# Kernel optimization log

Hardware: AMD Instinct MI355X
Metric: run time of the kernel (lower is better)

Reference implementation:

```python
import jax, jax.numpy as jnp
import numpy as np

B, V, FC, J = 1024, 5023, 9976, 5
NSHAPE, NEXP = 100, 50
PARENTS = np.array([-1, 0, 1, 1, 1])
NECK_CHAIN = np.array([1, 0])  # neck then its parent (global)


def batch_rodrigues(rv):
    # rv: [N,3] axis-angle -> [N,3,3] rotation matrices
    angle = jnp.linalg.norm(rv + 1e-8, axis=1, keepdims=True)  # [N,1]
    n = rv / angle
    rx, ry, rz = n[:, 0], n[:, 1], n[:, 2]
    z = jnp.zeros_like(rx)
    K = jnp.stack([z, -rz, ry, rz, z, -rx, -ry, rx, z], axis=1).reshape(-1, 3, 3)
    s = jnp.sin(angle)[..., None]
    c = jnp.cos(angle)[..., None]
    I = jnp.eye(3, dtype=rv.dtype)
    return I + s * K + (1.0 - c) * jnp.matmul(K, K)


def setup_inputs() -> dict:
    key = jax.random.key(0)
    ks = jax.random.split(key, 16)
    inp = {}
    inp["shape_params"] = jax.random.normal(ks[0], (B, NSHAPE), jnp.float32)
    inp["expression_params"] = jax.random.normal(ks[1], (B, NEXP), jnp.float32)
    inp["pose_params"] = jax.random.normal(ks[2], (B, 6), jnp.float32) * 0.2
    inp["v_template"] = jax.random.normal(ks[3], (V, 3), jnp.float32) * 0.1
    inp["shapedirs"] = jax.random.normal(ks[4], (V, 3, NSHAPE + NEXP), jnp.float32) * 0.01
    inp["posedirs"] = jax.random.normal(ks[5], (36, V * 3), jnp.float32) * 0.01
    Jr = jax.random.uniform(ks[6], (J, V), jnp.float32)
    inp["J_regressor"] = Jr / Jr.sum(1, keepdims=True)
    Wl = jax.random.uniform(ks[7], (V, J), jnp.float32)
    inp["lbs_weights"] = Wl / Wl.sum(1, keepdims=True)
    inp["neck_pose"] = jnp.zeros((1, 3), jnp.float32)
    inp["eye_pose"] = jnp.zeros((1, 6), jnp.float32)
    inp["faces"] = jax.random.randint(ks[8], (FC, 3), 0, V)
    inp["lmk_faces_idx"] = jax.random.randint(ks[9], (51,), 0, FC)
    b = jax.random.uniform(ks[10], (51, 3), jnp.float32)
    inp["lmk_bary_coords"] = b / b.sum(-1, keepdims=True)
    inp["dynamic_lmk_faces_idx"] = jax.random.randint(ks[11], (79, 17), 0, FC)
    db = jax.random.uniform(ks[12], (79, 17, 3), jnp.float32)
    inp["dynamic_lmk_bary_coords"] = db / db.sum(-1, keepdims=True)
    inp["full_lmk_faces_idx"] = jax.random.randint(ks[13], (68,), 0, FC)
    fb = jax.random.uniform(ks[14], (68, 3), jnp.float32)
    inp["full_lmk_bary_coords"] = fb / fb.sum(-1, keepdims=True)
    return inp


def reference(shape_params, expression_params, pose_params, v_template, shapedirs,
              posedirs, J_regressor, lbs_weights, neck_pose, eye_pose, faces,
              lmk_faces_idx, lmk_bary_coords, dynamic_lmk_faces_idx,
              dynamic_lmk_bary_coords, full_lmk_faces_idx, full_lmk_bary_coords):
    b = shape_params.shape[0]
    dt = shape_params.dtype
    betas = jnp.concatenate([shape_params, expression_params], 1)  # [B,150]
    full_pose = jnp.concatenate([pose_params[:, :3],
                                 jnp.broadcast_to(neck_pose, (b, 3)),
                                 pose_params[:, 3:],
                                 jnp.broadcast_to(eye_pose, (b, 6))], 1)  # [B,15]
    # shape/expression blendshapes
    v_shaped = v_template[None] + jnp.einsum('bl,vcl->bvc', betas, shapedirs)  # [B,V,3]
    joints = jnp.einsum('jv,bvc->bjc', J_regressor, v_shaped)  # [B,J,3]
    rot_mats = batch_rodrigues(full_pose.reshape(-1, 3)).reshape(b, J, 3, 3)
    ident = jnp.eye(3, dtype=dt)
    pose_feature = (rot_mats[:, 1:] - ident).reshape(b, -1)  # [B,36]
    v_posed = v_shaped + (pose_feature @ posedirs).reshape(b, V, 3)
    # kinematic chain of rigid transforms
    rel_joints = joints.at[:, 1:].add(-joints[:, PARENTS[1:]])
    tmat = jnp.concatenate([rot_mats, rel_joints[..., None]], -1)  # [B,J,3,4]
    bottom = jnp.broadcast_to(jnp.array([0., 0., 0., 1.], dt), (b, J, 1, 4))
    tmat = jnp.concatenate([tmat, bottom], 2)  # [B,J,4,4]
    chains = [tmat[:, 0]]
    for i in range(1, J):
        chains.append(chains[PARENTS[i]] @ tmat[:, i])
    transforms = jnp.stack(chains, 1)  # [B,J,4,4]
    joints_h = jnp.concatenate([joints, jnp.zeros((b, J, 1), dt)], -1)
    rel_tf = transforms - jnp.pad(transforms @ joints_h[..., None],
                                  ((0, 0), (0, 0), (0, 0), (3, 0)))
    # linear blend skinning
    T = jnp.einsum('vj,bjmn->bvmn', lbs_weights, rel_tf)  # [B,V,4,4]
    v_h = jnp.concatenate([v_posed, jnp.ones((b, V, 1), dt)], -1)
    vertices = jnp.einsum('bvmn,bvn->bvm', T, v_h)[..., :3]  # [B,V,3]
    # dynamic contour landmark selection via neck kinematic chain yaw
    aa = full_pose.reshape(b, J, 3)[:, NECK_CHAIN]  # [B,2,3]
    rch = batch_rodrigues(aa.reshape(-1, 3)).reshape(b, 2, 3, 3)
    rel_rot = rch[:, 1] @ rch[:, 0]  # loop order: R_global @ R_neck
    sy = jnp.sqrt(rel_rot[:, 0, 0] ** 2 + rel_rot[:, 1, 0] ** 2)
    yang = jnp.arctan2(-rel_rot[:, 2, 0], sy) * (180.0 / np.pi)
    y = jnp.round(jnp.minimum(yang, 39.0)).astype(jnp.int32)
    neg = y < 0
    big = y < -39
    y = jnp.where(neg, jnp.where(big, 78, 39 - y), y)
    dyn_faces = dynamic_lmk_faces_idx[y]   # [B,17]
    dyn_bary = dynamic_lmk_bary_coords[y]  # [B,17,3]
    lf = jnp.concatenate([dyn_faces,
                          jnp.broadcast_to(lmk_faces_idx[None], (b,) + lmk_faces_idx.shape)], 1)
    lb = jnp.concatenate([dyn_bary,
                          jnp.broadcast_to(lmk_bary_coords[None], (b,) + lmk_bary_coords.shape)], 1)

    def _lmk(verts, lfaces, lbary):
        tri = faces[lfaces]  # [B,L,3] vertex ids
        lv = jax.vmap(lambda v, t: v[t])(verts, tri)  # [B,L,3,3]
        return jnp.einsum('blfc,blf->blc', lv, lbary)

    landmarks2d = _lmk(vertices, lf, lb)  # [B,68,3]
    full_lf = jnp.broadcast_to(full_lmk_faces_idx[None], (b,) + full_lmk_faces_idx.shape)
    full_lb = jnp.broadcast_to(full_lmk_bary_coords[None], (b,) + full_lmk_bary_coords.shape)
    landmarks3d = _lmk(vertices, full_lf, full_lb)  # [B,68,3]
    return vertices, landmarks2d, landmarks3d
```

## Files before the change

kernel.cpp:

```cpp
#include <hip/hip_runtime.h>
#include <math.h>

#define BATCH 1024
#define NV 5023
#define NJ 5
#define K1 150
#define K2 36
#define KTOT 186
#define MCOLS (NV*3)
#define NCHUNK 80
#define CHUNKV 63

typedef __attribute__((ext_vector_type(4))) float floatx4;

#define WS_JSD     0
#define WS_RELTF   2272
#define WS_Y       63712
#define WS_AT      64736
#define WS_PARTIAL 64736

__device__ __forceinline__ void rodrigues(const float* rv, float* R) {
  const float ex = rv[0]+1e-8f, ey = rv[1]+1e-8f, ez = rv[2]+1e-8f;
  const float angle = sqrtf(ex*ex + ey*ey + ez*ez);
  const float inv = 1.0f/angle;
  const float nx = rv[0]*inv, ny = rv[1]*inv, nz = rv[2]*inv;
  const float s = sinf(angle), c = cosf(angle);
  const float omc = 1.0f - c;
  R[0] = 1.0f - omc*(ny*ny+nz*nz);
  R[1] = -s*nz + omc*nx*ny;
  R[2] =  s*ny + omc*nx*nz;
  R[3] =  s*nz + omc*nx*ny;
  R[4] = 1.0f - omc*(nx*nx+nz*nz);
  R[5] = -s*nx + omc*ny*nz;
  R[6] = -s*ny + omc*nx*nz;
  R[7] =  s*nx + omc*ny*nz;
  R[8] = 1.0f - omc*(nx*nx+ny*ny);
}

__launch_bounds__(512)
__global__ void k1_jsd_partial(const float* __restrict__ jreg, const float* __restrict__ shdirs,
                               const float* __restrict__ vtemp, float* __restrict__ partial) {
  const int chunk = blockIdx.x;
  const int t = threadIdx.x;
  if (t >= 453) return;
  const int v0 = chunk*CHUNKV;
  const int v1 = (v0 + CHUNKV < NV) ? v0 + CHUNKV : NV;
  float acc[5] = {0.f,0.f,0.f,0.f,0.f};
  if (t < 450) {
    for (int v = v0; v < v1; ++v) {
      const float sv = shdirs[(size_t)v*450 + t];
      #pragma unroll
      for (int j=0;j<5;++j) acc[j] = fmaf(jreg[j*NV + v], sv, acc[j]);
    }
  } else {
    const int c = t - 450;
    for (int v = v0; v < v1; ++v) {
      const float sv = vtemp[v*3 + c];
      #pragma unroll
      for (int j=0;j<5;++j) acc[j] = fmaf(jreg[j*NV + v], sv, acc[j]);
    }
  }
  #pragma unroll
  for (int j=0;j<5;++j)
    partial[(size_t)(chunk*NJ + j)*453 + t] = acc[j];
}

__launch_bounds__(256)
__global__ void k1b_jsd_reduce(const float* __restrict__ partial, float* __restrict__ jsd) {
  const int i = blockIdx.x*256 + threadIdx.x;
  if (i >= NJ*453) return;
  float s = 0.0f;
  for (int c = 0; c < NCHUNK; ++c) s += partial[(size_t)c*(NJ*453) + i];
  jsd[i] = s;
}

__launch_bounds__(256)
__global__ void k2_pose(const float* __restrict__ shape, const float* __restrict__ expr,
                        const float* __restrict__ pose, const float* __restrict__ neck,
                        const float* __restrict__ eye, const float* __restrict__ jsd,
                        float* __restrict__ At, float* __restrict__ reltf,
                        int* __restrict__ yidx) {
  const int b = blockIdx.x*256 + threadIdx.x;
  if (b >= BATCH) return;

  float fp[15];
  fp[0]=pose[b*6+0]; fp[1]=pose[b*6+1]; fp[2]=pose[b*6+2];
  fp[3]=neck[0];     fp[4]=neck[1];     fp[5]=neck[2];
  fp[6]=pose[b*6+3]; fp[7]=pose[b*6+4]; fp[8]=pose[b*6+5];
  #pragma unroll
  for (int i=0;i<6;++i) fp[9+i] = eye[i];

  float R[5][9];
  #pragma unroll
  for (int j=0;j<5;++j) rodrigues(&fp[j*3], R[j]);

  for (int l=0;l<100;++l) At[(size_t)l*BATCH + b] = shape[(size_t)b*100 + l];
  for (int l=0;l<50;++l)  At[(size_t)(100+l)*BATCH + b] = expr[(size_t)b*50 + l];
  #pragma unroll
  for (int jj=0;jj<4;++jj)
    #pragma unroll
    for (int rc=0;rc<9;++rc)
      At[(size_t)(K1 + jj*9 + rc)*BATCH + b] = R[1+jj][rc] - ((rc==0||rc==4||rc==8)?1.0f:0.0f);

  float jac[15];
  #pragma unroll
  for (int jc=0;jc<15;++jc) jac[jc] = jsd[(jc/3)*453 + 450 + (jc%3)];
  for (int l=0;l<150;++l) {
    const float bv = (l<100) ? shape[(size_t)b*100+l] : expr[(size_t)b*50 + (l-100)];
    #pragma unroll
    for (int jc=0;jc<15;++jc)
      jac[jc] = fmaf(jsd[(jc/3)*453 + (jc%3)*150 + l], bv, jac[jc]);
  }

  float C[5][12];
  #pragma unroll
  for (int r=0;r<3;++r) {
    C[0][r*4+0]=R[0][r*3+0]; C[0][r*4+1]=R[0][r*3+1]; C[0][r*4+2]=R[0][r*3+2];
    C[0][r*4+3]=jac[r];
  }
  const int par[5] = {-1,0,1,1,1};
  #pragma unroll
  for (int i=1;i<5;++i) {
    const int p = par[i];
    const float rj0 = jac[i*3+0]-jac[p*3+0];
    const float rj1 = jac[i*3+1]-jac[p*3+1];
    const float rj2 = jac[i*3+2]-jac[p*3+2];
    #pragma unroll
    for (int r=0;r<3;++r) {
      const float c0=C[p][r*4+0], c1=C[p][r*4+1], c2=C[p][r*4+2], c3=C[p][r*4+3];
      C[i][r*4+0] = c0*R[i][0] + c1*R[i][3] + c2*R[i][6];
      C[i][r*4+1] = c0*R[i][1] + c1*R[i][4] + c2*R[i][7];
      C[i][r*4+2] = c0*R[i][2] + c1*R[i][5] + c2*R[i][8];
      C[i][r*4+3] = c0*rj0 + c1*rj1 + c2*rj2 + c3;
    }
  }

  float* rt = reltf + (size_t)b*60;
  #pragma unroll
  for (int j=0;j<5;++j) {
    const float jx=jac[j*3+0], jy=jac[j*3+1], jz=jac[j*3+2];
    #pragma unroll
    for (int r=0;r<3;++r) {
      const float m0=C[j][r*4+0], m1=C[j][r*4+1], m2=C[j][r*4+2], m3=C[j][r*4+3];
      rt[j*12+r*4+0]=m0; rt[j*12+r*4+1]=m1; rt[j*12+r*4+2]=m2;
      rt[j*12+r*4+3]=m3 - (m0*jx + m1*jy + m2*jz);
    }
  }

  const float c00=R[1][0], c10=R[1][3], c20=R[1][6];
  const float r00 = R[0][0]*c00 + R[0][1]*c10 + R[0][2]*c20;
  const float r10 = R[0][3]*c00 + R[0][4]*c10 + R[0][5]*c20;
  const float r20 = R[0][6]*c00 + R[0][7]*c10 + R[0][8]*c20;
  const float sy = sqrtf(r00*r00 + r10*r10);
  const float yang = atan2f(-r20, sy) * 57.29577951308232f;
  int y = (int)rintf(fminf(yang, 39.0f));
  if (y < 0) y = (y < -39) ? 78 : (39 - y);
  yidx[b] = y;
}

template<int KL, bool POSE>
__device__ __forceinline__ void chunk_body(int k0, int t, int vl, int aoff, int m0,
    const float* __restrict__ At, const float* __restrict__ shdirs,
    const float* __restrict__ pdirs, float* shB,
    float (&acc)[2][8][3]) {
  __syncthreads();
  if (!POSE) {
    constexpr int Q = KL/2;
    constexpr int TOT = 384*Q;
    for (int i = t; i < TOT; i += 512) {
      const int q  = i % Q;
      const int ml = i / Q;
      const int v  = ml/3, c = ml - v*3;
      int m = m0 + ml; if (m > MCOLS-1) m = MCOLS-1;
      const float2 f = *reinterpret_cast<const float2*>(shdirs + (size_t)m*K1 + k0 + 2*q);
      shB[(2*q)*512 + v*4 + c]   = f.x;
      shB[(2*q+1)*512 + v*4 + c] = f.y;
    }
  } else {
    constexpr int TOT = 384*KL;
    for (int i = t; i < TOT; i += 512) {
      const int kk = i / 384;
      const int ml = i - kk*384;
      const int v  = ml/3, c = ml - v*3;
      int m = m0 + ml; if (m > MCOLS-1) m = MCOLS-1;
      shB[kk*512 + v*4 + c] = pdirs[(size_t)(k0 - K1 + kk)*MCOLS + m];
    }
  }
  __syncthreads();
  #pragma unroll 2
  for (int kk = 0; kk < KL; ++kk) {
    const float* ap = At + (size_t)(k0+kk)*BATCH + aoff;
    float as[8];
    #pragma unroll
    for (int i=0;i<8;++i) as[i] = ap[i];
    const floatx4 bv0 = *reinterpret_cast<const floatx4*>(shB + kk*512 + vl*4);
    const floatx4 bv1 = *reinterpret_cast<const floatx4*>(shB + kk*512 + 256 + vl*4);
    #pragma unroll
    for (int i=0;i<8;++i) {
      acc[0][i][0] = fmaf(as[i], bv0[0], acc[0][i][0]);
      acc[0][i][1] = fmaf(as[i], bv0[1], acc[0][i][1]);
      acc[0][i][2] = fmaf(as[i], bv0[2], acc[0][i][2]);
      acc[1][i][0] = fmaf(as[i], bv1[0], acc[1][i][0]);
      acc[1][i][1] = fmaf(as[i], bv1[1], acc[1][i][1]);
      acc[1][i][2] = fmaf(as[i], bv1[2], acc[1][i][2]);
    }
  }
}

__launch_bounds__(512)
__global__ void k3_valu(const float* __restrict__ At, const float* __restrict__ shdirs,
                        const float* __restrict__ pdirs, const float* __restrict__ vtemp,
                        const float* __restrict__ lbsw, const float* __restrict__ reltf,
                        float* __restrict__ vout) {
  __shared__ float shB[32*512];
  __shared__ float sRel[64*60];

  const int t  = threadIdx.x;
  const int vl = t & 63;
  const int bg = t >> 6;
  const int v0 = blockIdx.x * 128;
  const int b0 = blockIdx.y * 64;
  const int m0 = v0*3;
  const int aoff = __builtin_amdgcn_readfirstlane(b0 + bg*8);

  for (int i = t; i < 64*60; i += 512)
    sRel[i] = reltf[(size_t)b0*60 + i];

  float acc[2][8][3] = {};

  #pragma unroll 1
  for (int ch = 0; ch < 4; ++ch)
    chunk_body<32,false>(ch*32, t, vl, aoff, m0, At, shdirs, pdirs, shB, acc);
  chunk_body<22,false>(128, t, vl, aoff, m0, At, shdirs, pdirs, shB, acc);
  chunk_body<32,true >(150, t, vl, aoff, m0, At, shdirs, pdirs, shB, acc);
  chunk_body<4, true >(182, t, vl, aoff, m0, At, shdirs, pdirs, shB, acc);

  #pragma unroll
  for (int p=0;p<2;++p) {
    const int v = v0 + vl + p*64;
    if (v >= NV) continue;
    float w5[5];
    #pragma unroll
    for (int j=0;j<5;++j) w5[j] = lbsw[(size_t)v*5 + j];
    const float tx = vtemp[(size_t)v*3+0];
    const float ty = vtemp[(size_t)v*3+1];
    const float tz = vtemp[(size_t)v*3+2];
    #pragma unroll
    for (int i=0;i<8;++i) {
      const int bl = bg*8 + i;
      const float* rl = &sRel[bl*60];
      const float vx = acc[p][i][0]+tx, vy = acc[p][i][1]+ty, vz = acc[p][i][2]+tz;
      float o[3];
      #pragma unroll
      for (int r=0;r<3;++r) {
        float a0=0.f,a1=0.f,a2=0.f,a3=0.f;
        #pragma unroll
        for (int j=0;j<5;++j) {
          a0 = fmaf(w5[j], rl[j*12+r*4+0], a0);
          a1 = fmaf(w5[j], rl[j*12+r*4+1], a1);
          a2 = fmaf(w5[j], rl[j*12+r*4+2], a2);
          a3 = fmaf(w5[j], rl[j*12+r*4+3], a3);
        }
        o[r] = fmaf(a0, vx, fmaf(a1, vy, fmaf(a2, vz, a3)));
      }
      float* dst = vout + ((size_t)(b0+bl)*NV + v)*3;
      dst[0]=o[0]; dst[1]=o[1]; dst[2]=o[2];
    }
  }
}

__launch_bounds__(192)
__global__ void k4_landmarks(const float* __restrict__ verts, const int* __restrict__ faces,
                             const int* __restrict__ lmkf, const float* __restrict__ lmkb,
                             const int* __restrict__ dynf, const float* __restrict__ dynb,
                             const int* __restrict__ fullf, const float* __restrict__ fullb,
                             const int* __restrict__ yidx, float* __restrict__ out2d,
                             float* __restrict__ out3d) {
  const int b = blockIdx.x;
  const int t = threadIdx.x;
  if (t >= 136) return;
  const int which = t >= 68;
  const int i = which ? (t-68) : t;
  int fidx; float bw0,bw1,bw2;
  if (!which) {
    if (i < 17) {
      const int y = yidx[b];
      fidx = dynf[y*17 + i];
      const float* p = dynb + ((size_t)y*17 + i)*3;
      bw0=p[0]; bw1=p[1]; bw2=p[2];
    } else {
      fidx = lmkf[i-17];
      const float* p = lmkb + (size_t)(i-17)*3;
      bw0=p[0]; bw1=p[1]; bw2=p[2];
    }
  } else {
    fidx = fullf[i];
    const float* p = fullb + (size_t)i*3;
    bw0=p[0]; bw1=p[1]; bw2=p[2];
  }
  const int t0 = faces[fidx*3+0], t1 = faces[fidx*3+1], t2 = faces[fidx*3+2];
  const float* vb = verts + (size_t)b*NV*3;
  float* dst = (which ? out3d : out2d) + ((size_t)b*68 + i)*3;
  #pragma unroll
  for (int c=0;c<3;++c)
    dst[c] = vb[(size_t)t0*3+c]*bw0 + vb[(size_t)t1*3+c]*bw1 + vb[(size_t)t2*3+c]*bw2;
}

extern "C" void kernel_launch(void* const* d_in, const int* in_sizes, int n_in,
                              void* d_out, int out_size, void* d_ws, size_t ws_size,
                              hipStream_t stream) {
  const float* shape = (const float*)d_in[0];
  const float* expr  = (const float*)d_in[1];
  const float* pose  = (const float*)d_in[2];
  const float* vtemp = (const float*)d_in[3];
  const float* shdirs= (const float*)d_in[4];
  const float* pdirs = (const float*)d_in[5];
  const float* jreg  = (const float*)d_in[6];
  const float* lbsw  = (const float*)d_in[7];
  const float* neck  = (const float*)d_in[8];
  const float* eye   = (const float*)d_in[9];
  const int*   faces = (const int*)d_in[10];
  const int*   lmkf  = (const int*)d_in[11];
  const float* lmkb  = (const float*)d_in[12];
  const int*   dynf  = (const int*)d_in[13];
  const float* dynb  = (const float*)d_in[14];
  const int*   fullf = (const int*)d_in[15];
  const float* fullb = (const float*)d_in[16];

  float* wsf = (float*)d_ws;
  float* jsd     = wsf + WS_JSD;
  float* reltf   = wsf + WS_RELTF;
  int*   yidx    = (int*)(wsf + WS_Y);
  float* At      = wsf + WS_AT;
  float* partial = wsf + WS_PARTIAL;

  float* vout  = (float*)d_out;
  float* out2d = vout + (size_t)BATCH*NV*3;
  float* out3d = out2d + (size_t)BATCH*68*3;

  hipLaunchKernelGGL(k1_jsd_partial, dim3(NCHUNK), dim3(512), 0, stream,
                     jreg, shdirs, vtemp, partial);
  hipLaunchKernelGGL(k1b_jsd_reduce, dim3(9), dim3(256), 0, stream, partial, jsd);
  hipLaunchKernelGGL(k2_pose, dim3(4), dim3(256), 0, stream,
                     shape, expr, pose, neck, eye, jsd, At, reltf, yidx);
  hipLaunchKernelGGL(k3_valu, dim3((NV + 127)/128, BATCH/64), dim3(512), 0, stream,
                     At, shdirs, pdirs, vtemp, lbsw, reltf, vout);
  hipLaunchKernelGGL(k4_landmarks, dim3(BATCH), dim3(192), 0, stream,
                     vout, faces, lmkf, lmkb, dynf, dynb, fullf, fullb, yidx, out2d, out3d);
}
```

Before: 220.0 us.

## Retile vertex GEMM kernel to 64 vertices x 16 batches per thread

The main blendshape/LBS kernel now uses 256-thread blocks covering 64 vertices, with each thread handling one vertex across 16 batch rows instead of two vertices across 8. This shrinks shared memory (padded row stride, no staged rel-transform table), doubles the grid and adds a launch_bounds occupancy hint. The aim is better occupancy and fewer redundant shared-memory B loads. In exchange, each thread reads twice as many A scalars per k, and the skinning epilogue now reads the transforms straight from global memory.

```diff
diff --git a/kernel.cpp b/kernel.cpp
--- a/kernel.cpp
+++ b/kernel.cpp
@@ -158,75 +158,66 @@
   yidx[b] = y;
 }
 
+#define SROW 260
+
 template<int KL, bool POSE>
 __device__ __forceinline__ void chunk_body(int k0, int t, int vl, int aoff, int m0,
     const float* __restrict__ At, const float* __restrict__ shdirs,
-    const float* __restrict__ pdirs, float* shB,
-    float (&acc)[2][8][3]) {
+    const float* __restrict__ pdirs, float* shB, float (&acc)[16][3]) {
   __syncthreads();
   if (!POSE) {
     constexpr int Q = KL/2;
-    constexpr int TOT = 384*Q;
-    for (int i = t; i < TOT; i += 512) {
+    constexpr int TOT = 192*Q;
+    for (int i = t; i < TOT; i += 256) {
       const int q  = i % Q;
       const int ml = i / Q;
       const int v  = ml/3, c = ml - v*3;
       int m = m0 + ml; if (m > MCOLS-1) m = MCOLS-1;
       const float2 f = *reinterpret_cast<const float2*>(shdirs + (size_t)m*K1 + k0 + 2*q);
-      shB[(2*q)*512 + v*4 + c]   = f.x;
-      shB[(2*q+1)*512 + v*4 + c] = f.y;
+      shB[(2*q)*SROW + v*4 + c]   = f.x;
+      shB[(2*q+1)*SROW + v*4 + c] = f.y;
     }
   } else {
-    constexpr int TOT = 384*KL;
-    for (int i = t; i < TOT; i += 512) {
-      const int kk = i / 384;
-      const int ml = i - kk*384;
+    constexpr int TOT = 192*KL;
+    for (int i = t; i < TOT; i += 256) {
+      const int kk = i / 192;
+      const int ml = i - kk*192;
       const int v  = ml/3, c = ml - v*3;
       int m = m0 + ml; if (m > MCOLS-1) m = MCOLS-1;
-      shB[kk*512 + v*4 + c] = pdirs[(size_t)(k0 - K1 + kk)*MCOLS + m];
+      shB[kk*SROW + v*4 + c] = pdirs[(size_t)(k0 - K1 + kk)*MCOLS + m];
     }
   }
   __syncthreads();
   #pragma unroll 2
   for (int kk = 0; kk < KL; ++kk) {
     const float* ap = At + (size_t)(k0+kk)*BATCH + aoff;
-    float as[8];
-    #pragma unroll
-    for (int i=0;i<8;++i) as[i] = ap[i];
-    const floatx4 bv0 = *reinterpret_cast<const floatx4*>(shB + kk*512 + vl*4);
-    const floatx4 bv1 = *reinterpret_cast<const floatx4*>(shB + kk*512 + 256 + vl*4);
-    #pragma unroll
-    for (int i=0;i<8;++i) {
-      acc[0][i][0] = fmaf(as[i], bv0[0], acc[0][i][0]);
-      acc[0][i][1] = fmaf(as[i], bv0[1], acc[0][i][1]);
-      acc[0][i][2] = fmaf(as[i], bv0[2], acc[0][i][2]);
-      acc[1][i][0] = fmaf(as[i], bv1[0], acc[1][i][0]);
-      acc[1][i][1] = fmaf(as[i], bv1[1], acc[1][i][1]);
-      acc[1][i][2] = fmaf(as[i], bv1[2], acc[1][i][2]);
-    }
-  }
-}
-
-__launch_bounds__(512)
+    const floatx4 bv = *reinterpret_cast<const floatx4*>(shB + kk*SROW + vl*4);
+    #pragma unroll
+    for (int i=0;i<16;++i) {
+      const float ai = ap[i];
+      acc[i][0] = fmaf(ai, bv[0], acc[i][0]);
+      acc[i][1] = fmaf(ai, bv[1], acc[i][1]);
+      acc[i][2] = fmaf(ai, bv[2], acc[i][2]);
+    }
+  }
+}
+
+__launch_bounds__(256, 4)
 __global__ void k3_valu(const float* __restrict__ At, const float* __restrict__ shdirs,
                         const float* __restrict__ pdirs, const float* __restrict__ vtemp,
                         const float* __restrict__ lbsw, const float* __restrict__ reltf,
                         float* __restrict__ vout) {
-  __shared__ float shB[32*512];
-  __shared__ float sRel[64*60];
+  __shared__ float shB[32*SROW];
 
   const int t  = threadIdx.x;
   const int vl = t & 63;
   const int bg = t >> 6;
-  const int v0 = blockIdx.x * 128;
+  const int v0 = blockIdx.x * 64;
   const int b0 = blockIdx.y * 64;
   const int m0 = v0*3;
-  const int aoff = __builtin_amdgcn_readfirstlane(b0 + bg*8);
-
-  for (int i = t; i < 64*60; i += 512)
-    sRel[i] = reltf[(size_t)b0*60 + i];
-
-  float acc[2][8][3] = {};
+  const int aoff = __builtin_amdgcn_readfirstlane(b0 + bg*16);
+
+  float acc[16][3] = {};
 
   #pragma unroll 1
   for (int ch = 0; ch < 4; ++ch)
@@ -235,21 +226,18 @@
   chunk_body<32,true >(150, t, vl, aoff, m0, At, shdirs, pdirs, shB, acc);
   chunk_body<4, true >(182, t, vl, aoff, m0, At, shdirs, pdirs, shB, acc);
 
-  #pragma unroll
-  for (int p=0;p<2;++p) {
-    const int v = v0 + vl + p*64;
-    if (v >= NV) continue;
+  const int v = v0 + vl;
+  if (v < NV) {
     float w5[5];
     #pragma unroll
     for (int j=0;j<5;++j) w5[j] = lbsw[(size_t)v*5 + j];
     const float tx = vtemp[(size_t)v*3+0];
     const float ty = vtemp[(size_t)v*3+1];
     const float tz = vtemp[(size_t)v*3+2];
-    #pragma unroll
-    for (int i=0;i<8;++i) {
-      const int bl = bg*8 + i;
-      const float* rl = &sRel[bl*60];
-      const float vx = acc[p][i][0]+tx, vy = acc[p][i][1]+ty, vz = acc[p][i][2]+tz;
+    #pragma unroll 1
+    for (int i=0;i<16;++i) {
+      const float* rl = reltf + (size_t)(aoff + i)*60;
+      const float vx = acc[i][0]+tx, vy = acc[i][1]+ty, vz = acc[i][2]+tz;
       float o[3];
       #pragma unroll
       for (int r=0;r<3;++r) {
@@ -263,7 +251,7 @@
         }
         o[r] = fmaf(a0, vx, fmaf(a1, vy, fmaf(a2, vz, a3)));
       }
-      float* dst = vout + ((size_t)(b0+bl)*NV + v)*3;
+      float* dst = vout + ((size_t)(aoff + i)*NV + v)*3;
       dst[0]=o[0]; dst[1]=o[1]; dst[2]=o[2];
     }
   }
@@ -343,7 +331,7 @@
   hipLaunchKernelGGL(k1b_jsd_reduce, dim3(9), dim3(256), 0, stream, partial, jsd);
   hipLaunchKernelGGL(k2_pose, dim3(4), dim3(256), 0, stream,
                      shape, expr, pose, neck, eye, jsd, At, reltf, yidx);
-  hipLaunchKernelGGL(k3_valu, dim3((NV + 127)/128, BATCH/64), dim3(512), 0, stream,
+  hipLaunchKernelGGL(k3_valu, dim3((NV + 63)/64, BATCH/64), dim3(256), 0, stream,
                      At, shdirs, pdirs, vtemp, lbsw, reltf, vout);
   hipLaunchKernelGGL(k4_landmarks, dim3(BATCH), dim3(192), 0, stream,
                      vout, faces, lmkf, lmkb, dynf, dynb, fullf, fullb, yidx, out2d, out3d);
```

After: 308.3 us. 1.4x slower.
